# Kernel tuning notes

Measured on AMD Instinct MI355X. Metric: run time of the kernel, lower is better.

## Reference

```python
import jax, jax.numpy as jnp
import numpy as np

H = 16       # num heads
D = 128      # head_dim
R = 64       # d_rope_latent
HID = 2048   # hidden_size
DL = 512     # d_latent
EPS = 1e-6


def _rmsnorm(x, g):
    return x * jax.lax.rsqrt(jnp.mean(x * x, axis=-1, keepdims=True) + EPS) * g


def setup_inputs() -> dict:
    key = jax.random.key(0)
    ks = jax.random.split(key, 8)
    B, S = 2, 2048
    s = 0.02
    return {
        "x":   jax.random.normal(ks[0], (B, S, HID), jnp.float32),
        "Wq":  jax.random.normal(ks[1], (HID, H * D), jnp.float32) * s,
        "Wkv": jax.random.normal(ks[2], (HID, DL), jnp.float32) * s,
        "Wkr": jax.random.normal(ks[3], (DL, H * R), jnp.float32) * s,
        "Wkn": jax.random.normal(ks[4], (DL, H * (D - R)), jnp.float32) * s,
        "Wv":  jax.random.normal(ks[5], (DL, H * D), jnp.float32) * s,
        "Wo":  jax.random.normal(ks[6], (H * D, HID), jnp.float32) * s,
        "gq":  jnp.ones((D,), jnp.float32),
        "gk":  jnp.ones((D,), jnp.float32),
    }


def reference(x, Wq, Wkv, Wkr, Wkn, Wv, Wo, gq, gk):
    B, S, _ = x.shape
    # q projection + per-head RMSNorm
    q = _rmsnorm((x @ Wq).reshape(B, S, H, D), gq)          # [B,S,H,D]
    # low-rank KV latent
    lat = x @ Wkv                                            # [B,S,DL]
    kr = (lat @ Wkr).reshape(B, S, H, R)                     # rope part
    kn = (lat @ Wkn).reshape(B, S, H, D - R)                 # nope part
    # pos_encoding is None in source -> no rotation applied, just concat
    k = _rmsnorm(jnp.concatenate([kr, kn], axis=-1), gk)     # [B,S,H,D]
    v = (lat @ Wv).reshape(B, S, H, D)
    # causal SDPA
    scale = 1.0 / jnp.sqrt(jnp.float32(D))
    scores = jnp.einsum('bqhd,bkhd->bhqk', q, k) * scale     # [B,H,S,S]
    causal = jnp.tril(jnp.ones((S, S), bool))
    scores = jnp.where(causal, scores, jnp.float32(-1e30))
    p = jax.nn.softmax(scores, axis=-1)
    o = jnp.einsum('bhqk,bkhd->bqhd', p, v).reshape(B, S, H * D)
    return o @ Wo
```

## Files before the change

kernel.cpp:

```cpp
#include <hip/hip_runtime.h>
#include <cstdint>
#include <cstddef>

typedef short v8s __attribute__((ext_vector_type(8)));
typedef float v4f __attribute__((ext_vector_type(4)));

__device__ inline float bs2f(short s) {
    return __uint_as_float(((unsigned int)(unsigned short)s) << 16);
}
__device__ inline short f2bs(float f) {
    unsigned int u = __float_as_uint(f);
    unsigned int r = (u + 0x7fffu + ((u >> 16) & 1u)) >> 16;
    return (short)r;
}

#define MFMA(a, b, c) __builtin_amdgcn_mfma_f32_16x16x32_bf16((a), (b), (c), 0, 0, 0)

#define GLOAD_LDS16(g, l)                                                  \
    __builtin_amdgcn_global_load_lds(                                      \
        (const __attribute__((address_space(1))) void*)(g),                \
        (__attribute__((address_space(3))) void*)(l), 16, 0, 0)

__global__ __launch_bounds__(256) void prep(const float* __restrict__ x,
                                            short* __restrict__ xb,
                                            const float* __restrict__ Wq,
                                            const float* __restrict__ Wkv,
                                            const float* __restrict__ Wkr,
                                            const float* __restrict__ Wkn,
                                            const float* __restrict__ Wv,
                                            const float* __restrict__ Wo,
                                            short* __restrict__ WtA,
                                            short* __restrict__ WtB,
                                            short* __restrict__ Wot) {
    int blk = blockIdx.x;
    if (blk < 8192) {
        int i = (blk * 256 + threadIdx.x) * 4;
        float4 v = *(const float4*)(x + i);
        short r[4] = {f2bs(v.x), f2bs(v.y), f2bs(v.z), f2bs(v.w)};
        *(uint2*)(xb + i) = *(const uint2*)r;
        return;
    }
    blk -= 8192;
    const float* W;
    short* Wt;
    int K, N, bx, by;
    if (blk < 4096)      { W = Wq;  Wt = WtA;                      K = 2048; N = 2048; bx = blk & 63; by = blk >> 6; }
    else if (blk < 5120) { blk -= 4096; W = Wkv; Wt = WtA + (size_t)2048 * 2048; K = 2048; N = 512;  bx = blk & 15; by = blk >> 4; }
    else if (blk < 5632) { blk -= 5120; W = Wkr; Wt = WtB;                       K = 512;  N = 1024; bx = blk & 31; by = blk >> 5; }
    else if (blk < 6144) { blk -= 5632; W = Wkn; Wt = WtB + (size_t)1024 * 512;  K = 512;  N = 1024; bx = blk & 31; by = blk >> 5; }
    else if (blk < 7168) { blk -= 6144; W = Wv;  Wt = WtB + (size_t)2048 * 512;  K = 512;  N = 2048; bx = blk & 63; by = blk >> 6; }
    else                 { blk -= 7168; W = Wo;  Wt = Wot;                       K = 2048; N = 2048; bx = blk & 63; by = blk >> 6; }

    __shared__ float tile[32][33];
    const int tx = threadIdx.x & 31, ty = threadIdx.x >> 5;
    const int n0 = bx * 32, k0 = by * 32;
#pragma unroll
    for (int i = 0; i < 32; i += 8) tile[ty + i][tx] = W[(size_t)(k0 + ty + i) * N + n0 + tx];
    __syncthreads();
#pragma unroll
    for (int i = 0; i < 32; i += 8)
        Wt[(size_t)(n0 + ty + i) * K + k0 + tx] = f2bs(tile[tx][ty + i]);
}

__global__ __launch_bounds__(256) void gemm_bt(const short* __restrict__ A,
                                               const short* __restrict__ Bt,
                                               void* __restrict__ C0,
                                               void* __restrict__ C1,
                                               void* __restrict__ C2,
                                               int M, int N, int K, int mode,
                                               const float* __restrict__ g,
                                               float scale) {
    __shared__ short As[128 * 32];
    __shared__ short Bs[128 * 32];
    const int tid = threadIdx.x;
    const int lane = tid & 63, wave = tid >> 6;
    const int l16 = lane & 15, quad = lane >> 4;
    const int wm = (wave >> 1) * 64, wn = (wave & 1) * 64;

    const int gx = gridDim.x;
    const int nwg = gx * gridDim.y;
    const int wg = blockIdx.y * gx + blockIdx.x;
    const int cpx = nwg >> 3;
    const int swz = (wg & 7) * cpx + (wg >> 3);
    const int m0 = (swz / gx) * 128, n0 = (swz % gx) * 128;

    const v4f VZ = {0.f, 0.f, 0.f, 0.f};
    v4f acc[4][4];
#pragma unroll
    for (int i = 0; i < 4; i++)
#pragma unroll
        for (int j = 0; j < 4; j++) acc[i][j] = VZ;

    const int r0 = wave * 32 + (lane >> 2);
    const int r1 = r0 + 16;
    const int c0 = ((lane & 3) ^ ((r0 >> 1) & 3)) * 8;
    const int c1 = ((lane & 3) ^ ((r1 >> 1) & 3)) * 8;
    const short* aSrc0 = A + (size_t)(m0 + r0) * K + c0;
    const short* aSrc1 = A + (size_t)(m0 + r1) * K + c1;
    const short* bSrc0 = Bt + (size_t)(n0 + r0) * K + c0;
    const short* bSrc1 = Bt + (size_t)(n0 + r1) * K + c1;
    short* const ldsA0 = &As[(wave * 32) * 32];
    short* const ldsA1 = &As[(wave * 32 + 16) * 32];
    short* const ldsB0 = &Bs[(wave * 32) * 32];
    short* const ldsB1 = &Bs[(wave * 32 + 16) * 32];

    for (int kk = 0; kk < K; kk += 32) {
        __syncthreads();
        GLOAD_LDS16(aSrc0 + kk, ldsA0);
        GLOAD_LDS16(aSrc1 + kk, ldsA1);
        GLOAD_LDS16(bSrc0 + kk, ldsB0);
        GLOAD_LDS16(bSrc1 + kk, ldsB1);
        __syncthreads();

        v8s af[4], bfr[4];
#pragma unroll
        for (int t = 0; t < 4; t++) {
            const int ra = wm + t * 16 + l16;
            af[t] = *(const v8s*)(&As[ra * 32 + ((quad ^ ((ra >> 1) & 3)) * 8)]);
        }
#pragma unroll
        for (int t = 0; t < 4; t++) {
            const int rb = wn + t * 16 + l16;
            bfr[t] = *(const v8s*)(&Bs[rb * 32 + ((quad ^ ((rb >> 1) & 3)) * 8)]);
        }
#pragma unroll
        for (int i = 0; i < 4; i++)
#pragma unroll
            for (int j = 0; j < 4; j++) acc[i][j] = MFMA(af[i], bfr[j], acc[i][j]);
    }

    if (mode == 2) {
        if (n0 < 2048) {
            __syncthreads();
            float* red = (float*)As;
#pragma unroll
            for (int i = 0; i < 4; i++) {
#pragma unroll
                for (int r = 0; r < 4; r++) {
                    float ss2 = 0.f;
#pragma unroll
                    for (int j = 0; j < 4; j++) { float v = acc[i][j][r]; ss2 += v * v; }
#pragma unroll
                    for (int off2 = 1; off2 < 16; off2 <<= 1) ss2 += __shfl_xor(ss2, off2);
                    if (l16 == 0) red[(wm + i * 16 + quad * 4 + r) * 2 + (wn >> 6)] = ss2;
                }
            }
            __syncthreads();
            float gv[4];
#pragma unroll
            for (int j = 0; j < 4; j++) gv[j] = g[wn + j * 16 + l16];
#pragma unroll
            for (int i = 0; i < 4; i++) {
#pragma unroll
                for (int r = 0; r < 4; r++) {
                    const int rl = wm + i * 16 + quad * 4 + r;
                    const float rs =
                        rsqrtf((red[rl * 2] + red[rl * 2 + 1]) * (1.f / 128.f) + 1e-6f) * scale;
#pragma unroll
                    for (int j = 0; j < 4; j++)
                        ((short*)C0)[(size_t)(m0 + rl) * 2048 + n0 + wn + j * 16 + l16] =
                            f2bs(acc[i][j][r] * rs * gv[j]);
                }
            }
        } else {
#pragma unroll
            for (int i = 0; i < 4; i++)
#pragma unroll
                for (int r = 0; r < 4; r++) {
                    const int row = m0 + wm + i * 16 + quad * 4 + r;
#pragma unroll
                    for (int j = 0; j < 4; j++)
                        ((short*)C1)[(size_t)row * 512 + n0 - 2048 + wn + j * 16 + l16] =
                            f2bs(acc[i][j][r]);
                }
        }
        return;
    }

    if (mode == 3 && n0 >= 2048) {
        short* C = (short*)C2;
#pragma unroll
        for (int i = 0; i < 4; i++) {
            const int row = m0 + wm + i * 16 + quad * 4;
            const int bq = row >> 11, s = row & 2047;
            const int kt = s >> 6, key = s & 63;
#pragma unroll
            for (int j = 0; j < 4; j++) {
                const int col = n0 - 2048 + wn + j * 16 + l16;
                const int hh = col >> 7, d = col & 127;
                size_t base = ((size_t)((bq * 16 + hh) * 32 + kt) * 128 + d) * 64 + key;
                short pk[4];
#pragma unroll
                for (int r = 0; r < 4; r++) pk[r] = f2bs(acc[i][j][r]);
                *(uint2*)(C + base) = *(const uint2*)pk;
            }
        }
        return;
    }

    void* Cb = C0;
    int ld = N, coff = 0;
    if (mode == 3) {
        if (n0 < 1024) { Cb = C0; ld = 1024; coff = 0; }
        else           { Cb = C1; ld = 1024; coff = 1024; }
    }
#pragma unroll
    for (int i = 0; i < 4; i++) {
#pragma unroll
        for (int r = 0; r < 4; r++) {
            const int row = m0 + wm + i * 16 + quad * 4 + r;
#pragma unroll
            for (int j = 0; j < 4; j++) {
                const int col = n0 - coff + wn + j * 16 + l16;
                float v = acc[i][j][r];
                if (mode == 1) ((float*)Cb)[(size_t)row * ld + col] = v;
                else ((short*)Cb)[(size_t)row * ld + col] = f2bs(v);
            }
        }
    }
}

__global__ __launch_bounds__(256) void gemm_bt2x(const short* __restrict__ A,
                                                 const short* __restrict__ Bt,
                                                 void* __restrict__ C0,
                                                 void* __restrict__ C1,
                                                 int M, int N, int K, int mode,
                                                 const float* __restrict__ g,
                                                 float scale) {
    __shared__ short As[2 * 128 * 32];
    __shared__ short Bs[2 * 128 * 32];
    const int tid = threadIdx.x;
    const int lane = tid & 63, wave = tid >> 6;
    const int l16 = lane & 15, quad = lane >> 4;
    const int wm = (wave >> 1) * 64, wn = (wave & 1) * 64;

    const int gx = gridDim.x;
    const int nwg = gx * gridDim.y;
    const int wg = blockIdx.y * gx + blockIdx.x;
    const int cpx = nwg >> 3;
    const int swz = (wg & 7) * cpx + (wg >> 3);
    const int m0 = (swz / gx) * 128, n0 = (swz % gx) * 128;

    const v4f VZ = {0.f, 0.f, 0.f, 0.f};
    v4f acc[4][4];
#pragma unroll
    for (int i = 0; i < 4; i++)
#pragma unroll
        for (int j = 0; j < 4; j++) acc[i][j] = VZ;

    const int r0 = wave * 32 + (lane >> 2);
    const int r1 = r0 + 16;
    const int c0 = ((lane & 3) ^ ((r0 >> 1) & 3)) * 8;
    const int c1 = ((lane & 3) ^ ((r1 >> 1) & 3)) * 8;
    const short* aSrc0 = A + (size_t)(m0 + r0) * K + c0;
    const short* aSrc1 = A + (size_t)(m0 + r1) * K + c1;
    const short* bSrc0 = Bt + (size_t)(n0 + r0) * K + c0;
    const short* bSrc1 = Bt + (size_t)(n0 + r1) * K + c1;
    const int la0 = (wave * 32) * 32, la1 = (wave * 32 + 16) * 32;

    for (int kk = 0; kk < K; kk += 64) {
        __syncthreads();
        __builtin_amdgcn_sched_barrier(0);
#pragma unroll
        for (int p = 0; p < 2; p++) {
            const int ko = kk + p * 32, lo = p * 4096;
            GLOAD_LDS16(aSrc0 + ko, &As[lo + la0]);
            GLOAD_LDS16(aSrc1 + ko, &As[lo + la1]);
            GLOAD_LDS16(bSrc0 + ko, &Bs[lo + la0]);
            GLOAD_LDS16(bSrc1 + ko, &Bs[lo + la1]);
        }
        __builtin_amdgcn_sched_barrier(0);
        __syncthreads();

#pragma unroll
        for (int p = 0; p < 2; p++) {
            const int lo = p * 4096;
            v8s af[4], bfr[4];
#pragma unroll
            for (int t = 0; t < 4; t++) {
                const int ra = wm + t * 16 + l16;
                af[t] = *(const v8s*)(&As[lo + ra * 32 + ((quad ^ ((ra >> 1) & 3)) * 8)]);
            }
#pragma unroll
            for (int t = 0; t < 4; t++) {
                const int rb = wn + t * 16 + l16;
                bfr[t] = *(const v8s*)(&Bs[lo + rb * 32 + ((quad ^ ((rb >> 1) & 3)) * 8)]);
            }
#pragma unroll
            for (int i = 0; i < 4; i++)
#pragma unroll
                for (int j = 0; j < 4; j++) acc[i][j] = MFMA(af[i], bfr[j], acc[i][j]);
        }
    }

    if (mode == 2) {
        if (n0 < 2048) {
            __syncthreads();
            float* red = (float*)As;
#pragma unroll
            for (int i = 0; i < 4; i++) {
#pragma unroll
                for (int r = 0; r < 4; r++) {
                    float ss2 = 0.f;
#pragma unroll
                    for (int j = 0; j < 4; j++) { float v = acc[i][j][r]; ss2 += v * v; }
#pragma unroll
                    for (int off2 = 1; off2 < 16; off2 <<= 1) ss2 += __shfl_xor(ss2, off2);
                    if (l16 == 0) red[(wm + i * 16 + quad * 4 + r) * 2 + (wn >> 6)] = ss2;
                }
            }
            __syncthreads();
            float gv[4];
#pragma unroll
            for (int j = 0; j < 4; j++) gv[j] = g[wn + j * 16 + l16];
#pragma unroll
            for (int i = 0; i < 4; i++) {
#pragma unroll
                for (int r = 0; r < 4; r++) {
                    const int rl = wm + i * 16 + quad * 4 + r;
                    const float rs =
                        rsqrtf((red[rl * 2] + red[rl * 2 + 1]) * (1.f / 128.f) + 1e-6f) * scale;
#pragma unroll
                    for (int j = 0; j < 4; j++)
                        ((short*)C0)[(size_t)(m0 + rl) * 2048 + n0 + wn + j * 16 + l16] =
                            f2bs(acc[i][j][r] * rs * gv[j]);
                }
            }
        } else {
#pragma unroll
            for (int i = 0; i < 4; i++)
#pragma unroll
                for (int r = 0; r < 4; r++) {
                    const int row = m0 + wm + i * 16 + quad * 4 + r;
#pragma unroll
                    for (int j = 0; j < 4; j++)
                        ((short*)C1)[(size_t)row * 512 + n0 - 2048 + wn + j * 16 + l16] =
                            f2bs(acc[i][j][r]);
                }
        }
        return;
    }

#pragma unroll
    for (int i = 0; i < 4; i++) {
#pragma unroll
        for (int r = 0; r < 4; r++) {
            const int row = m0 + wm + i * 16 + quad * 4 + r;
#pragma unroll
            for (int j = 0; j < 4; j++)
                ((float*)C0)[(size_t)row * N + n0 + wn + j * 16 + l16] = acc[i][j][r];
        }
    }
}

__global__ __launch_bounds__(256) void rmsnorm_k(const short* __restrict__ KR,
                                                 const short* __restrict__ KN,
                                                 const float* __restrict__ g,
                                                 short* __restrict__ Y) {
    const int tid = threadIdx.x;
    const int rh = blockIdx.x * 32 + (tid >> 3);
    const int j = tid & 7;
    const size_t ibase = (size_t)blockIdx.x * 2048 + (size_t)tid * 8;
    v8s a = *(const v8s*)(KR + ibase);
    v8s c = *(const v8s*)(KN + ibase);
    float af[8], cf[8];
    float ss = 0.f;
#pragma unroll
    for (int t = 0; t < 8; t++) {
        af[t] = bs2f(a[t]);
        cf[t] = bs2f(c[t]);
        ss += af[t] * af[t] + cf[t] * cf[t];
    }
#pragma unroll
    for (int off = 1; off < 8; off <<= 1) ss += __shfl_xor(ss, off);
    const float rs = rsqrtf(ss * (1.f / 128.f) + 1e-6f);
    const int m = rh >> 4, h = rh & 15;
    const int b = m >> 11, s = m & 2047;
    const size_t obase = ((size_t)((b * 16 + h) * 32 + (s >> 6)) * 64 + (s & 63)) * 128;
    const float* gp = g + j * 8;
    v8s o0, o1;
#pragma unroll
    for (int t = 0; t < 8; t++) {
        o0[t] = f2bs(af[t] * rs * gp[t]);
        o1[t] = f2bs(cf[t] * rs * gp[64 + t]);
    }
    *(v8s*)(Y + obase + j * 8) = o0;
    *(v8s*)(Y + obase + 64 + j * 8) = o1;
}

#define PSTR 72

__global__ __launch_bounds__(256) void flash_attn(const short* __restrict__ Q,
                                                  const short* __restrict__ Kp,
                                                  const short* __restrict__ Vp,
                                                  short* __restrict__ O, int S) {
    __shared__ short Ks[64 * 128];
    __shared__ short Vs[128 * 64];
    __shared__ short Ps[4][16 * PSTR];

    const int lane = threadIdx.x & 63, w = threadIdx.x >> 6;
    const int l16 = lane & 15, quad = lane >> 4;
    const int blk = blockIdx.x;
    const int g = blk >> 3;
    const int bh = (blk & 7) * 4 + (g & 3);
    const int b = bh >> 4, h = bh & 15;
    const int qb = 31 - (g >> 2);
    const int q0 = qb * 64 + w * 16;

    const int koffE = (lane >> 4) * 128 + (((lane & 15) ^ (lane >> 4)) << 3);
    const int koffO = (lane >> 4) * 128 + (((lane & 15) ^ 4 ^ (lane >> 4)) << 3);
    const int voffc = (lane >> 3) * 64 + (((lane & 7) ^ (lane >> 3)) << 3);
    const int swz = (l16 & 7) * 8;

    v8s bq[4];
    {
        const size_t qbase = ((size_t)(b * S + q0 + l16) * 16 + h) * 128;
#pragma unroll
        for (int kc = 0; kc < 4; kc++)
            bq[kc] = *(const v8s*)(Q + qbase + kc * 32 + quad * 8);
    }

    const v4f VZ = {0.f, 0.f, 0.f, 0.f};
    v4f accO[8];
    v4f accL = VZ;
#pragma unroll
    for (int d = 0; d < 8; d++) accO[d] = VZ;

    const short o1 = 0x3F80;
    const v8s vones = {o1, o1, o1, o1, o1, o1, o1, o1};

    const short* const kbh = Kp + (size_t)(bh * 32) * 8192;
    const short* const vbh = Vp + (size_t)(bh * 32) * 8192;

    const int nkt = qb + 1;
    for (int kt = 0; kt < nkt; ++kt) {
        __syncthreads();
        {
            const short* kb = kbh + (size_t)kt * 8192;
            const short* vb = vbh + (size_t)kt * 8192;
            const int c0 = w * 4;
            GLOAD_LDS16(kb + (c0 + 0) * 512 + koffE, Ks + (c0 + 0) * 512);
            GLOAD_LDS16(kb + (c0 + 1) * 512 + koffO, Ks + (c0 + 1) * 512);
            GLOAD_LDS16(kb + (c0 + 2) * 512 + koffE, Ks + (c0 + 2) * 512);
            GLOAD_LDS16(kb + (c0 + 3) * 512 + koffO, Ks + (c0 + 3) * 512);
            GLOAD_LDS16(vb + (c0 + 0) * 512 + voffc, Vs + (c0 + 0) * 512);
            GLOAD_LDS16(vb + (c0 + 1) * 512 + voffc, Vs + (c0 + 1) * 512);
            GLOAD_LDS16(vb + (c0 + 2) * 512 + voffc, Vs + (c0 + 2) * 512);
            GLOAD_LDS16(vb + (c0 + 3) * 512 + voffc, Vs + (c0 + 3) * 512);
        }
        __syncthreads();

        v4f sc[4];
        __builtin_amdgcn_s_setprio(1);
#pragma unroll
        for (int nt = 0; nt < 4; nt++) {
            v8s ak[4];
            const int krow = (nt * 16 + l16) * 128;
#pragma unroll
            for (int kc = 0; kc < 4; kc++)
                ak[kc] = *(const v8s*)(Ks + krow + ((quad * 8 + kc * 32) ^ swz));
            v4f s = VZ;
#pragma unroll
            for (int kc = 0; kc < 4; kc++) s = MFMA(ak[kc], bq[kc], s);
            sc[nt] = s;
        }
        __builtin_amdgcn_s_setprio(0);

        if (kt == nkt - 1) {
            const int qrow = q0 + l16;
            const int k0 = kt * 64;
#pragma unroll
            for (int nt = 0; nt < 4; nt++)
#pragma unroll
                for (int r = 0; r < 4; r++)
                    if (k0 + nt * 16 + quad * 4 + r > qrow) sc[nt][r] = -1e30f;
        }

#pragma unroll
        for (int nt = 0; nt < 4; nt++) {
            short pk[4];
#pragma unroll
            for (int r = 0; r < 4; r++) {
                float p = exp2f(sc[nt][r] - 20.f);
                pk[r] = (short)(__float_as_uint(p) >> 16);
            }
            *(uint2*)(&Ps[w][l16 * PSTR + nt * 16 + quad * 4]) = *(const uint2*)pk;
        }

        v8s ap[2];
#pragma unroll
        for (int kc2 = 0; kc2 < 2; kc2++)
            ap[kc2] = *(const v8s*)(&Ps[w][l16 * PSTR + kc2 * 32 + quad * 8]);
        __builtin_amdgcn_s_setprio(1);
#pragma unroll
        for (int dt = 0; dt < 8; dt++) {
            const int vrow = (dt * 16 + l16) * 64;
#pragma unroll
            for (int kc2 = 0; kc2 < 2; kc2++) {
                v8s bv = *(const v8s*)(Vs + vrow + ((quad * 8 + kc2 * 32) ^ swz));
                accO[dt] = MFMA(ap[kc2], bv, accO[dt]);
            }
        }
#pragma unroll
        for (int kc2 = 0; kc2 < 2; kc2++) accL = MFMA(ap[kc2], vones, accL);
        __builtin_amdgcn_s_setprio(0);
    }

#pragma unroll
    for (int r = 0; r < 4; r++) {
        const int rl = quad * 4 + r;
        const int qg = q0 + rl;
        const float inv = 1.f / accL[r];
        const size_t obase = ((size_t)(b * S + qg) * 16 + h) * 128;
#pragma unroll
        for (int dt = 0; dt < 8; dt++)
            O[obase + dt * 16 + l16] = f2bs(accO[dt][r] * inv);
    }
}

extern "C" void kernel_launch(void* const* d_in, const int* in_sizes, int n_in,
                              void* d_out, int out_size, void* d_ws, size_t ws_size,
                              hipStream_t stream) {
    (void)in_sizes; (void)n_in; (void)out_size; (void)ws_size;
    const float* x   = (const float*)d_in[0];
    const float* Wq  = (const float*)d_in[1];
    const float* Wkv = (const float*)d_in[2];
    const float* Wkr = (const float*)d_in[3];
    const float* Wkn = (const float*)d_in[4];
    const float* Wv  = (const float*)d_in[5];
    const float* Wo  = (const float*)d_in[6];
    const float* gq  = (const float*)d_in[7];
    const float* gk  = (const float*)d_in[8];

    const int B = 2, S = 2048, HID = 2048;
    const int M = B * S;

    char* ws = (char*)d_ws;
    size_t off = 0;
    auto alloc = [&](size_t bytes) {
        char* p = ws + off;
        off += (bytes + 255) & ~(size_t)255;
        return p;
    };
    short* xb   = (short*)alloc((size_t)M * HID * 2);
    short* WtA  = (short*)alloc((size_t)2560 * 2048 * 2);
    short* WtB  = (short*)alloc((size_t)4096 * 512 * 2);
    short* Wot  = (short*)alloc((size_t)2048 * 2048 * 2);
    short* qb   = (short*)alloc((size_t)M * 2048 * 2);
    short* lat  = (short*)alloc((size_t)M * 512 * 2);
    short* krr  = (short*)alloc((size_t)M * 1024 * 2);
    short* knr  = (short*)alloc((size_t)M * 1024 * 2);
    short* Kp   = (short*)alloc((size_t)M * 2048 * 2);
    short* Vp   = (short*)alloc((size_t)M * 2048 * 2);
    short* ob   = (short*)alloc((size_t)M * 2048 * 2);

    prep<<<19456, 256, 0, stream>>>(x, xb, Wq, Wkv, Wkr, Wkn, Wv, Wo, WtA, WtB, Wot);

    gemm_bt2x<<<dim3(2560 / 128, M / 128), 256, 0, stream>>>(
        xb, WtA, qb, lat, M, 2560, 2048, 2, gq,
        0.08838834764831845f * 1.4426950408889634f);

    gemm_bt<<<dim3(4096 / 128, M / 128), 256, 0, stream>>>(
        lat, WtB, krr, knr, Vp, M, 4096, 512, 3, nullptr, 0.f);
    rmsnorm_k<<<(M * 16) / 32, 256, 0, stream>>>(krr, knr, gk, Kp);

    flash_attn<<<dim3(1024), 256, 0, stream>>>(qb, Kp, Vp, ob, S);

    gemm_bt2x<<<dim3(2048 / 128, M / 128), 256, 0, stream>>>(
        ob, Wot, d_out, nullptr, M, 2048, 2048, 1, nullptr, 0.f);
}
```

Baseline: 362.8 us.

## Software-pipeline GEMM and flash-attention loads with double/triple LDS buffering

The single-buffer gemm_bt becomes a double-buffered kernel that prefetches the next K slice while computing the current one. A new triple-buffered gemm_bt3 uses explicit vmcnt waits to keep two slices in flight, and it replaces gemm_bt2x for the Q/latent and output projections. Flash attention now double-buffers its K/V tiles so the next tile's global-to-LDS loads overlap with compute. The cost is more LDS per block, which may lower occupancy. The flash-attention loop relies on implicit waits before the barrier for the asynchronous LDS loads to finish.

Result: faster. 331.9 us (-8.5%).

```diff
diff --git a/kernel.cpp b/kernel.cpp
--- a/kernel.cpp
+++ b/kernel.cpp
@@ -70,163 +70,6 @@
                                                int M, int N, int K, int mode,
                                                const float* __restrict__ g,
                                                float scale) {
-    __shared__ short As[128 * 32];
-    __shared__ short Bs[128 * 32];
-    const int tid = threadIdx.x;
-    const int lane = tid & 63, wave = tid >> 6;
-    const int l16 = lane & 15, quad = lane >> 4;
-    const int wm = (wave >> 1) * 64, wn = (wave & 1) * 64;
-
-    const int gx = gridDim.x;
-    const int nwg = gx * gridDim.y;
-    const int wg = blockIdx.y * gx + blockIdx.x;
-    const int cpx = nwg >> 3;
-    const int swz = (wg & 7) * cpx + (wg >> 3);
-    const int m0 = (swz / gx) * 128, n0 = (swz % gx) * 128;
-
-    const v4f VZ = {0.f, 0.f, 0.f, 0.f};
-    v4f acc[4][4];
-#pragma unroll
-    for (int i = 0; i < 4; i++)
-#pragma unroll
-        for (int j = 0; j < 4; j++) acc[i][j] = VZ;
-
-    const int r0 = wave * 32 + (lane >> 2);
-    const int r1 = r0 + 16;
-    const int c0 = ((lane & 3) ^ ((r0 >> 1) & 3)) * 8;
-    const int c1 = ((lane & 3) ^ ((r1 >> 1) & 3)) * 8;
-    const short* aSrc0 = A + (size_t)(m0 + r0) * K + c0;
-    const short* aSrc1 = A + (size_t)(m0 + r1) * K + c1;
-    const short* bSrc0 = Bt + (size_t)(n0 + r0) * K + c0;
-    const short* bSrc1 = Bt + (size_t)(n0 + r1) * K + c1;
-    short* const ldsA0 = &As[(wave * 32) * 32];
-    short* const ldsA1 = &As[(wave * 32 + 16) * 32];
-    short* const ldsB0 = &Bs[(wave * 32) * 32];
-    short* const ldsB1 = &Bs[(wave * 32 + 16) * 32];
-
-    for (int kk = 0; kk < K; kk += 32) {
-        __syncthreads();
-        GLOAD_LDS16(aSrc0 + kk, ldsA0);
-        GLOAD_LDS16(aSrc1 + kk, ldsA1);
-        GLOAD_LDS16(bSrc0 + kk, ldsB0);
-        GLOAD_LDS16(bSrc1 + kk, ldsB1);
-        __syncthreads();
-
-        v8s af[4], bfr[4];
-#pragma unroll
-        for (int t = 0; t < 4; t++) {
-            const int ra = wm + t * 16 + l16;
-            af[t] = *(const v8s*)(&As[ra * 32 + ((quad ^ ((ra >> 1) & 3)) * 8)]);
-        }
-#pragma unroll
-        for (int t = 0; t < 4; t++) {
-            const int rb = wn + t * 16 + l16;
-            bfr[t] = *(const v8s*)(&Bs[rb * 32 + ((quad ^ ((rb >> 1) & 3)) * 8)]);
-        }
-#pragma unroll
-        for (int i = 0; i < 4; i++)
-#pragma unroll
-            for (int j = 0; j < 4; j++) acc[i][j] = MFMA(af[i], bfr[j], acc[i][j]);
-    }
-
-    if (mode == 2) {
-        if (n0 < 2048) {
-            __syncthreads();
-            float* red = (float*)As;
-#pragma unroll
-            for (int i = 0; i < 4; i++) {
-#pragma unroll
-                for (int r = 0; r < 4; r++) {
-                    float ss2 = 0.f;
-#pragma unroll
-                    for (int j = 0; j < 4; j++) { float v = acc[i][j][r]; ss2 += v * v; }
-#pragma unroll
-                    for (int off2 = 1; off2 < 16; off2 <<= 1) ss2 += __shfl_xor(ss2, off2);
-                    if (l16 == 0) red[(wm + i * 16 + quad * 4 + r) * 2 + (wn >> 6)] = ss2;
-                }
-            }
-            __syncthreads();
-            float gv[4];
-#pragma unroll
-            for (int j = 0; j < 4; j++) gv[j] = g[wn + j * 16 + l16];
-#pragma unroll
-            for (int i = 0; i < 4; i++) {
-#pragma unroll
-                for (int r = 0; r < 4; r++) {
-                    const int rl = wm + i * 16 + quad * 4 + r;
-                    const float rs =
-                        rsqrtf((red[rl * 2] + red[rl * 2 + 1]) * (1.f / 128.f) + 1e-6f) * scale;
-#pragma unroll
-                    for (int j = 0; j < 4; j++)
-                        ((short*)C0)[(size_t)(m0 + rl) * 2048 + n0 + wn + j * 16 + l16] =
-                            f2bs(acc[i][j][r] * rs * gv[j]);
-                }
-            }
-        } else {
-#pragma unroll
-            for (int i = 0; i < 4; i++)
-#pragma unroll
-                for (int r = 0; r < 4; r++) {
-                    const int row = m0 + wm + i * 16 + quad * 4 + r;
-#pragma unroll
-                    for (int j = 0; j < 4; j++)
-                        ((short*)C1)[(size_t)row * 512 + n0 - 2048 + wn + j * 16 + l16] =
-                            f2bs(acc[i][j][r]);
-                }
-        }
-        return;
-    }
-
-    if (mode == 3 && n0 >= 2048) {
-        short* C = (short*)C2;
-#pragma unroll
-        for (int i = 0; i < 4; i++) {
-            const int row = m0 + wm + i * 16 + quad * 4;
-            const int bq = row >> 11, s = row & 2047;
-            const int kt = s >> 6, key = s & 63;
-#pragma unroll
-            for (int j = 0; j < 4; j++) {
-                const int col = n0 - 2048 + wn + j * 16 + l16;
-                const int hh = col >> 7, d = col & 127;
-                size_t base = ((size_t)((bq * 16 + hh) * 32 + kt) * 128 + d) * 64 + key;
-                short pk[4];
-#pragma unroll
-                for (int r = 0; r < 4; r++) pk[r] = f2bs(acc[i][j][r]);
-                *(uint2*)(C + base) = *(const uint2*)pk;
-            }
-        }
-        return;
-    }
-
-    void* Cb = C0;
-    int ld = N, coff = 0;
-    if (mode == 3) {
-        if (n0 < 1024) { Cb = C0; ld = 1024; coff = 0; }
-        else           { Cb = C1; ld = 1024; coff = 1024; }
-    }
-#pragma unroll
-    for (int i = 0; i < 4; i++) {
-#pragma unroll
-        for (int r = 0; r < 4; r++) {
-            const int row = m0 + wm + i * 16 + quad * 4 + r;
-#pragma unroll
-            for (int j = 0; j < 4; j++) {
-                const int col = n0 - coff + wn + j * 16 + l16;
-                float v = acc[i][j][r];
-                if (mode == 1) ((float*)Cb)[(size_t)row * ld + col] = v;
-                else ((short*)Cb)[(size_t)row * ld + col] = f2bs(v);
-            }
-        }
-    }
-}
-
-__global__ __launch_bounds__(256) void gemm_bt2x(const short* __restrict__ A,
-                                                 const short* __restrict__ Bt,
-                                                 void* __restrict__ C0,
-                                                 void* __restrict__ C1,
-                                                 int M, int N, int K, int mode,
-                                                 const float* __restrict__ g,
-                                                 float scale) {
     __shared__ short As[2 * 128 * 32];
     __shared__ short Bs[2 * 128 * 32];
     const int tid = threadIdx.x;
@@ -258,39 +101,219 @@
     const short* bSrc1 = Bt + (size_t)(n0 + r1) * K + c1;
     const int la0 = (wave * 32) * 32, la1 = (wave * 32 + 16) * 32;
 
-    for (int kk = 0; kk < K; kk += 64) {
+    GLOAD_LDS16(aSrc0, &As[la0]);
+    GLOAD_LDS16(aSrc1, &As[la1]);
+    GLOAD_LDS16(bSrc0, &Bs[la0]);
+    GLOAD_LDS16(bSrc1, &Bs[la1]);
+
+    int cur = 0;
+    for (int kk = 0; kk < K; kk += 32) {
         __syncthreads();
         __builtin_amdgcn_sched_barrier(0);
-#pragma unroll
-        for (int p = 0; p < 2; p++) {
-            const int ko = kk + p * 32, lo = p * 4096;
-            GLOAD_LDS16(aSrc0 + ko, &As[lo + la0]);
-            GLOAD_LDS16(aSrc1 + ko, &As[lo + la1]);
-            GLOAD_LDS16(bSrc0 + ko, &Bs[lo + la0]);
-            GLOAD_LDS16(bSrc1 + ko, &Bs[lo + la1]);
+        if (kk + 32 < K) {
+            const int lo = (cur ^ 1) * 4096;
+            GLOAD_LDS16(aSrc0 + kk + 32, &As[lo + la0]);
+            GLOAD_LDS16(aSrc1 + kk + 32, &As[lo + la1]);
+            GLOAD_LDS16(bSrc0 + kk + 32, &Bs[lo + la0]);
+            GLOAD_LDS16(bSrc1 + kk + 32, &Bs[lo + la1]);
         }
         __builtin_amdgcn_sched_barrier(0);
-        __syncthreads();
-
-#pragma unroll
-        for (int p = 0; p < 2; p++) {
-            const int lo = p * 4096;
-            v8s af[4], bfr[4];
-#pragma unroll
-            for (int t = 0; t < 4; t++) {
-                const int ra = wm + t * 16 + l16;
-                af[t] = *(const v8s*)(&As[lo + ra * 32 + ((quad ^ ((ra >> 1) & 3)) * 8)]);
-            }
-#pragma unroll
-            for (int t = 0; t < 4; t++) {
-                const int rb = wn + t * 16 + l16;
-                bfr[t] = *(const v8s*)(&Bs[lo + rb * 32 + ((quad ^ ((rb >> 1) & 3)) * 8)]);
-            }
+
+        const int lo = cur * 4096;
+        v8s af[4], bfr[4];
+#pragma unroll
+        for (int t = 0; t < 4; t++) {
+            const int ra = wm + t * 16 + l16;
+            af[t] = *(const v8s*)(&As[lo + ra * 32 + ((quad ^ ((ra >> 1) & 3)) * 8)]);
+        }
+#pragma unroll
+        for (int t = 0; t < 4; t++) {
+            const int rb = wn + t * 16 + l16;
+            bfr[t] = *(const v8s*)(&Bs[lo + rb * 32 + ((quad ^ ((rb >> 1) & 3)) * 8)]);
+        }
+#pragma unroll
+        for (int i = 0; i < 4; i++)
+#pragma unroll
+            for (int j = 0; j < 4; j++) acc[i][j] = MFMA(af[i], bfr[j], acc[i][j]);
+        cur ^= 1;
+    }
+
+    if (mode == 2) {
+        if (n0 < 2048) {
+            __syncthreads();
+            float* red = (float*)As;
+#pragma unroll
+            for (int i = 0; i < 4; i++) {
+#pragma unroll
+                for (int r = 0; r < 4; r++) {
+                    float ss2 = 0.f;
+#pragma unroll
+                    for (int j = 0; j < 4; j++) { float v = acc[i][j][r]; ss2 += v * v; }
+#pragma unroll
+                    for (int off2 = 1; off2 < 16; off2 <<= 1) ss2 += __shfl_xor(ss2, off2);
+                    if (l16 == 0) red[(wm + i * 16 + quad * 4 + r) * 2 + (wn >> 6)] = ss2;
+                }
+            }
+            __syncthreads();
+            float gv[4];
+#pragma unroll
+            for (int j = 0; j < 4; j++) gv[j] = g[wn + j * 16 + l16];
+#pragma unroll
+            for (int i = 0; i < 4; i++) {
+#pragma unroll
+                for (int r = 0; r < 4; r++) {
+                    const int rl = wm + i * 16 + quad * 4 + r;
+                    const float rs =
+                        rsqrtf((red[rl * 2] + red[rl * 2 + 1]) * (1.f / 128.f) + 1e-6f) * scale;
+#pragma unroll
+                    for (int j = 0; j < 4; j++)
+                        ((short*)C0)[(size_t)(m0 + rl) * 2048 + n0 + wn + j * 16 + l16] =
+                            f2bs(acc[i][j][r] * rs * gv[j]);
+                }
+            }
+        } else {
 #pragma unroll
             for (int i = 0; i < 4; i++)
 #pragma unroll
-                for (int j = 0; j < 4; j++) acc[i][j] = MFMA(af[i], bfr[j], acc[i][j]);
-        }
+                for (int r = 0; r < 4; r++) {
+                    const int row = m0 + wm + i * 16 + quad * 4 + r;
+#pragma unroll
+                    for (int j = 0; j < 4; j++)
+                        ((short*)C1)[(size_t)row * 512 + n0 - 2048 + wn + j * 16 + l16] =
+                            f2bs(acc[i][j][r]);
+                }
+        }
+        return;
+    }
+
+    if (mode == 3 && n0 >= 2048) {
+        short* C = (short*)C2;
+#pragma unroll
+        for (int i = 0; i < 4; i++) {
+            const int row = m0 + wm + i * 16 + quad * 4;
+            const int bq = row >> 11, s = row & 2047;
+            const int kt = s >> 6, key = s & 63;
+#pragma unroll
+            for (int j = 0; j < 4; j++) {
+                const int col = n0 - 2048 + wn + j * 16 + l16;
+                const int hh = col >> 7, d = col & 127;
+                size_t base = ((size_t)((bq * 16 + hh) * 32 + kt) * 128 + d) * 64 + key;
+                short pk[4];
+#pragma unroll
+                for (int r = 0; r < 4; r++) pk[r] = f2bs(acc[i][j][r]);
+                *(uint2*)(C + base) = *(const uint2*)pk;
+            }
+        }
+        return;
+    }
+
+    void* Cb = C0;
+    int ld = N, coff = 0;
+    if (mode == 3) {
+        if (n0 < 1024) { Cb = C0; ld = 1024; coff = 0; }
+        else           { Cb = C1; ld = 1024; coff = 1024; }
+    }
+#pragma unroll
+    for (int i = 0; i < 4; i++) {
+#pragma unroll
+        for (int r = 0; r < 4; r++) {
+            const int row = m0 + wm + i * 16 + quad * 4 + r;
+#pragma unroll
+            for (int j = 0; j < 4; j++) {
+                const int col = n0 - coff + wn + j * 16 + l16;
+                float v = acc[i][j][r];
+                if (mode == 1) ((float*)Cb)[(size_t)row * ld + col] = v;
+                else ((short*)Cb)[(size_t)row * ld + col] = f2bs(v);
+            }
+        }
+    }
+}
+
+__global__ __launch_bounds__(256) void gemm_bt3(const short* __restrict__ A,
+                                                const short* __restrict__ Bt,
+                                                void* __restrict__ C0,
+                                                void* __restrict__ C1,
+                                                int M, int N, int K, int mode,
+                                                const float* __restrict__ g,
+                                                float scale) {
+    __shared__ short As[3 * 128 * 32];
+    __shared__ short Bs[3 * 128 * 32];
+    const int tid = threadIdx.x;
+    const int lane = tid & 63, wave = tid >> 6;
+    const int l16 = lane & 15, quad = lane >> 4;
+    const int wm = (wave >> 1) * 64, wn = (wave & 1) * 64;
+
+    const int gx = gridDim.x;
+    const int nwg = gx * gridDim.y;
+    const int wg = blockIdx.y * gx + blockIdx.x;
+    const int cpx = nwg >> 3;
+    const int swz = (wg & 7) * cpx + (wg >> 3);
+    const int m0 = (swz / gx) * 128, n0 = (swz % gx) * 128;
+
+    const v4f VZ = {0.f, 0.f, 0.f, 0.f};
+    v4f acc[4][4];
+#pragma unroll
+    for (int i = 0; i < 4; i++)
+#pragma unroll
+        for (int j = 0; j < 4; j++) acc[i][j] = VZ;
+
+    const int r0 = wave * 32 + (lane >> 2);
+    const int r1 = r0 + 16;
+    const int c0 = ((lane & 3) ^ ((r0 >> 1) & 3)) * 8;
+    const int c1 = ((lane & 3) ^ ((r1 >> 1) & 3)) * 8;
+    const short* aSrc0 = A + (size_t)(m0 + r0) * K + c0;
+    const short* aSrc1 = A + (size_t)(m0 + r1) * K + c1;
+    const short* bSrc0 = Bt + (size_t)(n0 + r0) * K + c0;
+    const short* bSrc1 = Bt + (size_t)(n0 + r1) * K + c1;
+    const int la0 = (wave * 32) * 32, la1 = (wave * 32 + 16) * 32;
+
+    GLOAD_LDS16(aSrc0, &As[la0]);
+    GLOAD_LDS16(aSrc1, &As[la1]);
+    GLOAD_LDS16(bSrc0, &Bs[la0]);
+    GLOAD_LDS16(bSrc1, &Bs[la1]);
+    GLOAD_LDS16(aSrc0 + 32, &As[4096 + la0]);
+    GLOAD_LDS16(aSrc1 + 32, &As[4096 + la1]);
+    GLOAD_LDS16(bSrc0 + 32, &Bs[4096 + la0]);
+    GLOAD_LDS16(bSrc1 + 32, &Bs[4096 + la1]);
+
+    int cur = 0;
+    for (int kk = 0; kk < K; kk += 32) {
+        if (kk + 32 < K) {
+            asm volatile("s_waitcnt vmcnt(4)" ::: "memory");
+        } else {
+            asm volatile("s_waitcnt vmcnt(0)" ::: "memory");
+        }
+        __builtin_amdgcn_sched_barrier(0);
+        __builtin_amdgcn_s_barrier();
+        __builtin_amdgcn_sched_barrier(0);
+
+        if (kk + 64 < K) {
+            const int nb = cur + 2 >= 3 ? cur - 1 : cur + 2;
+            const int lo = nb * 4096;
+            GLOAD_LDS16(aSrc0 + kk + 64, &As[lo + la0]);
+            GLOAD_LDS16(aSrc1 + kk + 64, &As[lo + la1]);
+            GLOAD_LDS16(bSrc0 + kk + 64, &Bs[lo + la0]);
+            GLOAD_LDS16(bSrc1 + kk + 64, &Bs[lo + la1]);
+        }
+        __builtin_amdgcn_sched_barrier(0);
+
+        const int lo = cur * 4096;
+        v8s af[4], bfr[4];
+#pragma unroll
+        for (int t = 0; t < 4; t++) {
+            const int ra = wm + t * 16 + l16;
+            af[t] = *(const v8s*)(&As[lo + ra * 32 + ((quad ^ ((ra >> 1) & 3)) * 8)]);
+        }
+#pragma unroll
+        for (int t = 0; t < 4; t++) {
+            const int rb = wn + t * 16 + l16;
+            bfr[t] = *(const v8s*)(&Bs[lo + rb * 32 + ((quad ^ ((rb >> 1) & 3)) * 8)]);
+        }
+#pragma unroll
+        for (int i = 0; i < 4; i++)
+#pragma unroll
+            for (int j = 0; j < 4; j++) acc[i][j] = MFMA(af[i], bfr[j], acc[i][j]);
+        cur = cur + 1 >= 3 ? 0 : cur + 1;
     }
 
     if (mode == 2) {
@@ -394,8 +417,8 @@
                                                   const short* __restrict__ Kp,
                                                   const short* __restrict__ Vp,
                                                   short* __restrict__ O, int S) {
-    __shared__ short Ks[64 * 128];
-    __shared__ short Vs[128 * 64];
+    __shared__ short Ks[2][64 * 128];
+    __shared__ short Vs[2][128 * 64];
     __shared__ short Ps[4][16 * PSTR];
 
     const int lane = threadIdx.x & 63, w = threadIdx.x >> 6;
@@ -412,6 +435,10 @@
     const int voffc = (lane >> 3) * 64 + (((lane & 7) ^ (lane >> 3)) << 3);
     const int swz = (l16 & 7) * 8;
 
+    const short* const kbh = Kp + (size_t)(bh * 32) * 8192;
+    const short* const vbh = Vp + (size_t)(bh * 32) * 8192;
+    const int c0 = w * 4;
+
     v8s bq[4];
     {
         const size_t qbase = ((size_t)(b * S + q0 + l16) * 16 + h) * 128;
@@ -429,26 +456,43 @@
     const short o1 = 0x3F80;
     const v8s vones = {o1, o1, o1, o1, o1, o1, o1, o1};
 
-    const short* const kbh = Kp + (size_t)(bh * 32) * 8192;
-    const short* const vbh = Vp + (size_t)(bh * 32) * 8192;
-
     const int nkt = qb + 1;
+
+    {
+        const short* kb = kbh;
+        const short* vb = vbh;
+        GLOAD_LDS16(kb + (c0 + 0) * 512 + koffE, &Ks[0][(c0 + 0) * 512]);
+        GLOAD_LDS16(kb + (c0 + 1) * 512 + koffO, &Ks[0][(c0 + 1) * 512]);
+        GLOAD_LDS16(kb + (c0 + 2) * 512 + koffE, &Ks[0][(c0 + 2) * 512]);
+        GLOAD_LDS16(kb + (c0 + 3) * 512 + koffO, &Ks[0][(c0 + 3) * 512]);
+        GLOAD_LDS16(vb + (c0 + 0) * 512 + voffc, &Vs[0][(c0 + 0) * 512]);
+        GLOAD_LDS16(vb + (c0 + 1) * 512 + voffc, &Vs[0][(c0 + 1) * 512]);
+        GLOAD_LDS16(vb + (c0 + 2) * 512 + voffc, &Vs[0][(c0 + 2) * 512]);
+        GLOAD_LDS16(vb + (c0 + 3) * 512 + voffc, &Vs[0][(c0 + 3) * 512]);
+    }
+
+    int cur = 0;
     for (int kt = 0; kt < nkt; ++kt) {
         __syncthreads();
-        {
-            const short* kb = kbh + (size_t)kt * 8192;
-            const short* vb = vbh + (size_t)kt * 8192;
-            const int c0 = w * 4;
-            GLOAD_LDS16(kb + (c0 + 0) * 512 + koffE, Ks + (c0 + 0) * 512);
-            GLOAD_LDS16(kb + (c0 + 1) * 512 + koffO, Ks + (c0 + 1) * 512);
-            GLOAD_LDS16(kb + (c0 + 2) * 512 + koffE, Ks + (c0 + 2) * 512);
-            GLOAD_LDS16(kb + (c0 + 3) * 512 + koffO, Ks + (c0 + 3) * 512);
-            GLOAD_LDS16(vb + (c0 + 0) * 512 + voffc, Vs + (c0 + 0) * 512);
-            GLOAD_LDS16(vb + (c0 + 1) * 512 + voffc, Vs + (c0 + 1) * 512);
-            GLOAD_LDS16(vb + (c0 + 2) * 512 + voffc, Vs + (c0 + 2) * 512);
-            GLOAD_LDS16(vb + (c0 + 3) * 512 + voffc, Vs + (c0 + 3) * 512);
-        }
-        __syncthreads();
+        __builtin_amdgcn_sched_barrier(0);
+        if (kt + 1 < nkt) {
+            const short* kb = kbh + (size_t)(kt + 1) * 8192;
+            const short* vb = vbh + (size_t)(kt + 1) * 8192;
+            short* ksd = &Ks[cur ^ 1][0];
+            short* vsd = &Vs[cur ^ 1][0];
+            GLOAD_LDS16(kb + (c0 + 0) * 512 + koffE, ksd + (c0 + 0) * 512);
+            GLOAD_LDS16(kb + (c0 + 1) * 512 + koffO, ksd + (c0 + 1) * 512);
+            GLOAD_LDS16(kb + (c0 + 2) * 512 + koffE, ksd + (c0 + 2) * 512);
+            GLOAD_LDS16(kb + (c0 + 3) * 512 + koffO, ksd + (c0 + 3) * 512);
+            GLOAD_LDS16(vb + (c0 + 0) * 512 + voffc, vsd + (c0 + 0) * 512);
+            GLOAD_LDS16(vb + (c0 + 1) * 512 + voffc, vsd + (c0 + 1) * 512);
+            GLOAD_LDS16(vb + (c0 + 2) * 512 + voffc, vsd + (c0 + 2) * 512);
+            GLOAD_LDS16(vb + (c0 + 3) * 512 + voffc, vsd + (c0 + 3) * 512);
+        }
+        __builtin_amdgcn_sched_barrier(0);
+
+        const short* const ksr = &Ks[cur][0];
+        const short* const vsr = &Vs[cur][0];
 
         v4f sc[4];
         __builtin_amdgcn_s_setprio(1);
@@ -458,7 +502,7 @@
             const int krow = (nt * 16 + l16) * 128;
 #pragma unroll
             for (int kc = 0; kc < 4; kc++)
-                ak[kc] = *(const v8s*)(Ks + krow + ((quad * 8 + kc * 32) ^ swz));
+                ak[kc] = *(const v8s*)(ksr + krow + ((quad * 8 + kc * 32) ^ swz));
             v4f s = VZ;
 #pragma unroll
             for (int kc = 0; kc < 4; kc++) s = MFMA(ak[kc], bq[kc], s);
@@ -497,13 +541,14 @@
             const int vrow = (dt * 16 + l16) * 64;
 #pragma unroll
             for (int kc2 = 0; kc2 < 2; kc2++) {
-                v8s bv = *(const v8s*)(Vs + vrow + ((quad * 8 + kc2 * 32) ^ swz));
+                v8s bv = *(const v8s*)(vsr + vrow + ((quad * 8 + kc2 * 32) ^ swz));
                 accO[dt] = MFMA(ap[kc2], bv, accO[dt]);
             }
         }
 #pragma unroll
         for (int kc2 = 0; kc2 < 2; kc2++) accL = MFMA(ap[kc2], vones, accL);
         __builtin_amdgcn_s_setprio(0);
+        cur ^= 1;
     }
 
 #pragma unroll
@@ -556,7 +601,7 @@
 
     prep<<<19456, 256, 0, stream>>>(x, xb, Wq, Wkv, Wkr, Wkn, Wv, Wo, WtA, WtB, Wot);
 
-    gemm_bt2x<<<dim3(2560 / 128, M / 128), 256, 0, stream>>>(
+    gemm_bt3<<<dim3(2560 / 128, M / 128), 256, 0, stream>>>(
         xb, WtA, qb, lat, M, 2560, 2048, 2, gq,
         0.08838834764831845f * 1.4426950408889634f);
 
@@ -566,6 +611,6 @@
 
     flash_attn<<<dim3(1024), 256, 0, stream>>>(qb, Kp, Vp, ob, S);
 
-    gemm_bt2x<<<dim3(2048 / 128, M / 128), 256, 0, stream>>>(
+    gemm_bt3<<<dim3(2048 / 128, M / 128), 256, 0, stream>>>(
         ob, Wot, d_out, nullptr, M, 2048, 2048, 1, nullptr, 0.f);
 }
```
